# Kernel tuning notes

Hardware: AMD Instinct MI355X
Metric: run time of the kernel (lower is better)

Reference implementation:

```python
import jax, jax.numpy as jnp
import numpy as np

B, T, IN, D = 32, 1024, 1536, 768


def setup_inputs() -> dict:
    key = jax.random.key(0)
    ks = jax.random.split(key, 14)
    s_in = 1.0 / np.sqrt(IN)
    s_d = 1.0 / np.sqrt(D)
    return {
        "x": jax.random.normal(ks[0], (B, T, IN), jnp.float32),
        # fc1/fc2 torch Linear weights stored [out, in]
        "fc1_w": jax.random.normal(ks[1], (IN, IN), jnp.float32) * s_in,
        "fc1_b": jax.random.normal(ks[2], (IN,), jnp.float32) * 0.01,
        "fc2_w": jax.random.normal(ks[3], (D, IN), jnp.float32) * s_in,
        "fc2_b": jax.random.normal(ks[4], (D,), jnp.float32) * 0.01,
        # Unary: Conv1d(D,D,k=1) then Conv1d(D,1,k=1); k=1 conv == per-token linear
        "un_emb_w": jax.random.normal(ks[5], (D, D), jnp.float32) * s_d,
        "un_emb_b": jax.random.normal(ks[6], (D,), jnp.float32) * 0.01,
        "un_red_w": jax.random.normal(ks[7], (1, D), jnp.float32) * s_d,
        "un_red_b": jax.random.normal(ks[8], (1,), jnp.float32) * 0.01,
        # Self Pairwise: x_embedding / y_embedding Conv1d(D,D,k=1)
        "pw_x_w": jax.random.normal(ks[9], (D, D), jnp.float32) * s_d,
        "pw_x_b": jax.random.normal(ks[10], (D,), jnp.float32) * 0.01,
        "pw_y_w": jax.random.normal(ks[11], (D, D), jnp.float32) * s_d,
        "pw_y_b": jax.random.normal(ks[12], (D,), jnp.float32) * 0.01,
        # reduce_potentials: Conv1d(2,1,k=1,bias=False) -> 2 scalars
        "red_w": jax.random.normal(ks[13], (2,), jnp.float32),
    }


def reference(x, fc1_w, fc1_b, fc2_w, fc2_b,
              un_emb_w, un_emb_b, un_red_w, un_red_b,
              pw_x_w, pw_x_b, pw_y_w, pw_y_b, red_w):
    # FGAEmbedder MLP: fc2(relu(fc1(x)))
    h = jax.nn.relu(jnp.einsum('bti,oi->bto', x, fc1_w) + fc1_b)
    u = jnp.einsum('bti,oi->bto', h, fc2_w) + fc2_b            # [B,T,D]

    # Unary potential (dropout is identity at inference)
    e = jax.nn.relu(jnp.einsum('btd,od->bto', u, un_emb_w) + un_emb_b)
    un_pot = (jnp.einsum('btd,od->bto', e, un_red_w) + un_red_b)[..., 0]  # [B,T]

    # Self pairwise: cosine-similarity matrix, marginalized by mean (spatial_dim=None)
    xe = jnp.einsum('btd,od->bto', u, pw_x_w) + pw_x_b
    ye = jnp.einsum('btd,od->bto', u, pw_y_w) + pw_y_b
    xn = xe / jnp.maximum(jnp.linalg.norm(xe, axis=-1, keepdims=True), 1e-12)
    yn = ye / jnp.maximum(jnp.linalg.norm(ye, axis=-1, keepdims=True), 1e-12)
    S = jnp.einsum('btd,bsd->bts', xn, yn)                     # [B,T,T]
    pw_pot = jnp.mean(S, axis=2)                               # [B,T]

    # reduce potentials (Conv1d 2->1 no bias; order: unary then self), softmax attention
    scores = red_w[0] * un_pot + red_w[1] * pw_pot             # [B,T]
    w = jax.nn.softmax(scores, axis=1)
    return jnp.einsum('btd,bt->bd', u, w)                      # [B,D]
```

## Files before the change

### kernel.cpp

```cpp
#include <hip/hip_runtime.h>
#include <stdint.h>

#define MROWS 32768
#define TSEQ  1024
#define BBATCH 32
#define INDIM 1536
#define DDIM  768
#define NCAT  2304

typedef short short8 __attribute__((ext_vector_type(8)));
typedef short short4v __attribute__((ext_vector_type(4)));
typedef float f32x4  __attribute__((ext_vector_type(4)));

__device__ __forceinline__ float b2f(ushort u) {
    union { uint32_t u; float f; } x; x.u = ((uint32_t)u) << 16; return x.f;
}
__device__ __forceinline__ ushort f2b(float f) {
    union { float f; uint32_t u; } x; x.f = f;
    uint32_t r = x.u + 0x7fffu + ((x.u >> 16) & 1u);
    return (ushort)(r >> 16);
}

__device__ __forceinline__ void cvt4(const float* __restrict__ in, ushort* __restrict__ out, int i) {
    float4 v = ((const float4*)in)[i];
    ushort4 o;
    o.x = f2b(v.x); o.y = f2b(v.y); o.z = f2b(v.z); o.w = f2b(v.w);
    ((ushort4*)out)[i] = o;
}

#define C0 12582912
#define C1 13172736
#define C2 13467648
#define C3 13615104
#define C4 13762560
#define C5 13910016
#define C6 13910592
#define C7 13916736
#define C8 13922880
#define C9 13947456
__global__ void cvt_all(const float* __restrict__ x,
                        const float* __restrict__ fc1_w, const float* __restrict__ fc2_w,
                        const float* __restrict__ w3a, const float* __restrict__ w3b,
                        const float* __restrict__ w3c,
                        const float* __restrict__ ba, const float* __restrict__ bb,
                        const float* __restrict__ bc,
                        ushort* __restrict__ X16, ushort* __restrict__ W1,
                        ushort* __restrict__ W2, ushort* __restrict__ W3,
                        float* __restrict__ B3, float* __restrict__ ybar_z,
                        float* __restrict__ out_z, float* __restrict__ stats_z)
{
    int i = blockIdx.x * 256 + threadIdx.x;
    float4 z = {0.f, 0.f, 0.f, 0.f};
    if (i < C0)       cvt4(x, X16, i);
    else if (i < C1)  cvt4(fc1_w, W1, i - C0);
    else if (i < C2)  cvt4(fc2_w, W2, i - C1);
    else if (i < C3)  cvt4(w3a, W3,           i - C2);
    else if (i < C4)  cvt4(w3b, W3 + 589824,  i - C3);
    else if (i < C5)  cvt4(w3c, W3 + 1179648, i - C4);
    else if (i < C6) {
        int j = i - C5;
        const float* src = (j < 192) ? ba : (j < 384) ? bb : bc;
        int off = (j < 192) ? j : (j < 384) ? (j - 192) : (j - 384);
        ((float4*)B3)[j] = ((const float4*)src)[off];
    }
    else if (i < C7)  ((float4*)ybar_z)[i - C6] = z;
    else if (i < C8)  ((float4*)out_z)[i - C7] = z;
    else if (i < C9)  ((float4*)stats_z)[i - C8] = z;
}

__global__ __launch_bounds__(256, 2)
void gemm_bt(const ushort* __restrict__ A, const ushort* __restrict__ Bm,
             const float* __restrict__ bias, ushort* __restrict__ C,
             int M, int N, int K, int relu_ncols,
             const float* __restrict__ urw, float* __restrict__ SE,
             float* __restrict__ SX, float* __restrict__ SY)
{
    __shared__ __align__(16) ushort lA[128 * 64];
    __shared__ __align__(16) ushort lB[128 * 64];

    const int tid  = threadIdx.x;
    const int lane = tid & 63, wave = tid >> 6;
    const int wm = wave & 1, wn = wave >> 1;
    const int quad = lane >> 4, r16 = lane & 15;

    const int ntiles = N >> 7;
    const int xcd = blockIdx.x & 7;
    const int j   = blockIdx.x >> 3;
    const int g   = j / ntiles;
    const int n_t = j - g * ntiles;
    const int m_t = xcd + (g << 3);
    const int m0 = m_t * 128, n0 = n_t * 128;

    const int srow = lane >> 2;
    const int scol = ((lane & 3) ^ ((lane >> 3) & 3)) * 8;
    const int goff = (r16 << 5) + ((quad ^ ((r16 >> 1) & 3)) << 3);

    f32x4 acc[4][4] = {};

    const int kIters = K >> 6;
    for (int kt = 0; kt < kIters; ++kt) {
        const int k0 = kt << 6;
        __syncthreads();
#pragma unroll
        for (int c = 0; c < 4; ++c) {
            int S  = wave * 4 + c;
            int kh = S >> 3, rs = S & 7;
            int row = rs * 16 + srow;
            int kc  = k0 + kh * 32 + scol;
            const ushort* ga = A + (size_t)(m0 + row) * K + kc;
            __builtin_amdgcn_global_load_lds(
                (const __attribute__((address_space(1))) void*)ga,
                (__attribute__((address_space(3))) void*)&lA[S * 512], 16, 0, 0);
            const ushort* gb = Bm + (size_t)(n0 + row) * K + kc;
            __builtin_amdgcn_global_load_lds(
                (const __attribute__((address_space(1))) void*)gb,
                (__attribute__((address_space(3))) void*)&lB[S * 512], 16, 0, 0);
        }
        __syncthreads();

#pragma unroll
        for (int kh = 0; kh < 2; ++kh) {
            short8 af[4], bf[4];
#pragma unroll
            for (int i = 0; i < 4; ++i)
                af[i] = *(const short8*)&lA[kh * 4096 + (wm * 4 + i) * 512 + goff];
#pragma unroll
            for (int j2 = 0; j2 < 4; ++j2)
                bf[j2] = *(const short8*)&lB[kh * 4096 + (wn * 4 + j2) * 512 + goff];
#pragma unroll
            for (int i = 0; i < 4; ++i)
#pragma unroll
                for (int j2 = 0; j2 < 4; ++j2)
                    acc[i][j2] = __builtin_amdgcn_mfma_f32_16x16x32_bf16(af[i], bf[j2], acc[i][j2], 0, 0, 0);
        }
    }

    const bool stats = (urw != nullptr);
    const int sec = n0 / DDIM;
    float st[4][4] = {};
#pragma unroll
    for (int j2 = 0; j2 < 4; ++j2) {
        int gn = n0 + wn * 64 + j2 * 16 + r16;
        float bv = bias[gn];
        bool dorelu = gn < relu_ncols;
        float uw = (stats && sec == 0) ? urw[gn] : 0.f;
#pragma unroll
        for (int i = 0; i < 4; ++i) {
            int gmb = m0 + wm * 64 + i * 16 + quad * 4;
#pragma unroll
            for (int rr = 0; rr < 4; ++rr) {
                float v = acc[i][j2][rr] + bv;
                if (dorelu) v = fmaxf(v, 0.f);
                C[(size_t)(gmb + rr) * N + gn] = f2b(v);
                if (stats) st[i][rr] += (sec == 0) ? v * uw : v * v;
            }
        }
    }
    if (stats) {
#pragma unroll
        for (int i = 0; i < 4; ++i)
#pragma unroll
            for (int rr = 0; rr < 4; ++rr) {
                float v = st[i][rr];
                v += __shfl_xor(v, 1, 64);
                v += __shfl_xor(v, 2, 64);
                v += __shfl_xor(v, 4, 64);
                v += __shfl_xor(v, 8, 64);
                st[i][rr] = v;
            }
        if (r16 == 0) {
            float* dst = (sec == 0) ? SE : (sec == 1) ? SX : SY;
#pragma unroll
            for (int i = 0; i < 4; ++i)
#pragma unroll
                for (int rr = 0; rr < 4; ++rr)
                    atomicAdd(&dst[m0 + wm * 64 + i * 16 + quad * 4 + rr], st[i][rr]);
        }
    }
}

__global__ void ybar_k(const ushort* __restrict__ G3, const float* __restrict__ sy,
                       float* __restrict__ ybar)
{
    int b = blockIdx.x, s0 = blockIdx.y * 32;
    int tid = threadIdx.x;
    __shared__ float sr[32];
    if (tid < 32) {
        float v = sy[b * TSEQ + s0 + tid];
        sr[tid] = (1.0f / TSEQ) / fmaxf(sqrtf(v), 1e-12f);
    }
    __syncthreads();
    float a0 = 0.f, a1 = 0.f, a2 = 0.f;
#pragma unroll 8
    for (int s = 0; s < 32; ++s) {
        const ushort* row = G3 + (size_t)(b * TSEQ + s0 + s) * NCAT + 2 * DDIM;
        float w = sr[s];
        a0 += b2f(row[tid])       * w;
        a1 += b2f(row[tid + 256]) * w;
        a2 += b2f(row[tid + 512]) * w;
    }
    atomicAdd(&ybar[b * DDIM + tid],       a0);
    atomicAdd(&ybar[b * DDIM + tid + 256], a1);
    atomicAdd(&ybar[b * DDIM + tid + 512], a2);
}

__global__ void pw_scores_k(const ushort* __restrict__ G3, const float* __restrict__ ybar,
                            const float* __restrict__ SE, const float* __restrict__ SX,
                            const float* __restrict__ urb, const float* __restrict__ red_w,
                            float* __restrict__ scores)
{
    int wv = threadIdx.x >> 6, lane = threadIdx.x & 63;
    int m = blockIdx.x * 4 + wv;
    int b = m >> 10;
    const ushort* xe = G3 + (size_t)m * NCAT + DDIM;
    const float4* yb = (const float4*)(ybar + b * DDIM);
    float s = 0.f;
#pragma unroll
    for (int c0 = 0; c0 < 3; ++c0) {
        int c = lane + c0 * 64;
        short4v v = *(const short4v*)(xe + c * 4);
        float4 yv = yb[c];
        s += b2f((ushort)v[0]) * yv.x + b2f((ushort)v[1]) * yv.y
           + b2f((ushort)v[2]) * yv.z + b2f((ushort)v[3]) * yv.w;
    }
#pragma unroll
    for (int off = 32; off; off >>= 1) s += __shfl_xor(s, off, 64);
    if (lane == 0) {
        float rnx = 1.f / fmaxf(sqrtf(SX[m]), 1e-12f);
        scores[m] = red_w[0] * (SE[m] + urb[0]) + red_w[1] * (rnx * s);
    }
}

__global__ void out_sm_k(const ushort* __restrict__ U16, const float* __restrict__ scores,
                         float* __restrict__ out)
{
    int b = blockIdx.x, t0 = blockIdx.y * 32;
    int tid = threadIdx.x;
    int lane = tid & 63, wv = tid >> 6;
    __shared__ float red[8];
    __shared__ float sw[32];

    float v[4];
    float lm = -1e30f;
#pragma unroll
    for (int i = 0; i < 4; ++i) {
        v[i] = scores[b * TSEQ + i * 256 + tid];
        lm = fmaxf(lm, v[i]);
    }
#pragma unroll
    for (int off = 32; off; off >>= 1) lm = fmaxf(lm, __shfl_xor(lm, off, 64));
    if (lane == 0) red[wv] = lm;
    __syncthreads();
    float smax = fmaxf(fmaxf(red[0], red[1]), fmaxf(red[2], red[3]));
    float ls = 0.f;
#pragma unroll
    for (int i = 0; i < 4; ++i) ls += expf(v[i] - smax);
#pragma unroll
    for (int off = 32; off; off >>= 1) ls += __shfl_xor(ls, off, 64);
    if (lane == 0) red[4 + wv] = ls;
    __syncthreads();
    float inv = 1.f / (red[4] + red[5] + red[6] + red[7]);

    if (tid < 32) sw[tid] = expf(scores[b * TSEQ + t0 + tid] - smax) * inv;
    __syncthreads();

    float a0 = 0.f, a1 = 0.f, a2 = 0.f;
#pragma unroll 8
    for (int t = 0; t < 32; ++t) {
        const ushort* row = U16 + (size_t)(b * TSEQ + t0 + t) * DDIM;
        float w = sw[t];
        a0 += b2f(row[tid])       * w;
        a1 += b2f(row[tid + 256]) * w;
        a2 += b2f(row[tid + 512]) * w;
    }
    atomicAdd(&out[b * DDIM + tid],       a0);
    atomicAdd(&out[b * DDIM + tid + 256], a1);
    atomicAdd(&out[b * DDIM + tid + 512], a2);
}

static const size_t O_X16   = 0;
static const size_t O_H16   = 100663296;
static const size_t O_G3    = 0;
static const size_t O_U16   = 201326592;
static const size_t O_W1    = 251658240;
static const size_t O_W2    = 256376832;
static const size_t O_W3    = 258736128;
static const size_t O_B3    = 262275072;
static const size_t O_SE    = 262284288;
static const size_t O_SX    = 262415360;
static const size_t O_SY    = 262546432;
static const size_t O_SCORE = 262677504;
static const size_t O_YBAR  = 262939648;

extern "C" void kernel_launch(void* const* d_in, const int* in_sizes, int n_in,
                              void* d_out, int out_size, void* d_ws, size_t ws_size,
                              hipStream_t stream)
{
    const float* x        = (const float*)d_in[0];
    const float* fc1_w    = (const float*)d_in[1];
    const float* fc1_b    = (const float*)d_in[2];
    const float* fc2_w    = (const float*)d_in[3];
    const float* fc2_b    = (const float*)d_in[4];
    const float* un_emb_w = (const float*)d_in[5];
    const float* un_emb_b = (const float*)d_in[6];
    const float* un_red_w = (const float*)d_in[7];
    const float* un_red_b = (const float*)d_in[8];
    const float* pw_x_w   = (const float*)d_in[9];
    const float* pw_x_b   = (const float*)d_in[10];
    const float* pw_y_w   = (const float*)d_in[11];
    const float* pw_y_b   = (const float*)d_in[12];
    const float* red_w    = (const float*)d_in[13];

    char* ws = (char*)d_ws;
    ushort* X16 = (ushort*)(ws + O_X16);
    ushort* H16 = (ushort*)(ws + O_H16);
    ushort* G3  = (ushort*)(ws + O_G3);
    ushort* U16 = (ushort*)(ws + O_U16);
    ushort* W1  = (ushort*)(ws + O_W1);
    ushort* W2  = (ushort*)(ws + O_W2);
    ushort* W3  = (ushort*)(ws + O_W3);
    float*  B3  = (float*)(ws + O_B3);
    float*  SE  = (float*)(ws + O_SE);
    float*  SX  = (float*)(ws + O_SX);
    float*  SY  = (float*)(ws + O_SY);
    float*  SCORES = (float*)(ws + O_SCORE);
    float*  YBAR = (float*)(ws + O_YBAR);

    cvt_all<<<54483, 256, 0, stream>>>(x, fc1_w, fc2_w, un_emb_w, pw_x_w, pw_y_w,
                                       un_emb_b, pw_x_b, pw_y_b,
                                       X16, W1, W2, W3, B3, YBAR, (float*)d_out, SE);

    gemm_bt<<<(MROWS / 128) * (INDIM / 128), 256, 0, stream>>>(
        X16, W1, fc1_b, H16, MROWS, INDIM, INDIM, INDIM,
        nullptr, nullptr, nullptr, nullptr);
    gemm_bt<<<(MROWS / 128) * (DDIM / 128), 256, 0, stream>>>(
        H16, W2, fc2_b, U16, MROWS, DDIM, INDIM, 0,
        nullptr, nullptr, nullptr, nullptr);
    gemm_bt<<<(MROWS / 128) * (NCAT / 128), 256, 0, stream>>>(
        U16, W3, B3, G3, MROWS, NCAT, DDIM, DDIM,
        un_red_w, SE, SX, SY);

    ybar_k<<<dim3(BBATCH, 32), 256, 0, stream>>>(G3, SY, YBAR);
    pw_scores_k<<<MROWS / 4, 256, 0, stream>>>(G3, YBAR, SE, SX, un_red_b, red_w, SCORES);
    out_sm_k<<<dim3(BBATCH, 32), 256, 0, stream>>>(U16, SCORES, (float*)d_out);
}
```

Before: 726.7 us.

## Use 256x256 GEMM tiles with 4-stage LDS prefetch pipeline

```diff
diff --git a/kernel.cpp b/kernel.cpp
--- a/kernel.cpp
+++ b/kernel.cpp
@@ -68,88 +68,122 @@
     else if (i < C9)  ((float4*)stats_z)[i - C8] = z;
 }
 
-__global__ __launch_bounds__(256, 2)
+__global__ __launch_bounds__(512, 2)
 void gemm_bt(const ushort* __restrict__ A, const ushort* __restrict__ Bm,
              const float* __restrict__ bias, ushort* __restrict__ C,
              int M, int N, int K, int relu_ncols,
              const float* __restrict__ urw, float* __restrict__ SE,
              float* __restrict__ SX, float* __restrict__ SY)
 {
-    __shared__ __align__(16) ushort lA[128 * 64];
-    __shared__ __align__(16) ushort lB[128 * 64];
+    __shared__ __align__(16) ushort lds[65536];
 
     const int tid  = threadIdx.x;
     const int lane = tid & 63, wave = tid >> 6;
-    const int wm = wave & 1, wn = wave >> 1;
+    const int wm = wave >> 2, wn = wave & 3;
     const int quad = lane >> 4, r16 = lane & 15;
 
-    const int ntiles = N >> 7;
+    const int ntiles = N >> 8;
     const int xcd = blockIdx.x & 7;
     const int j   = blockIdx.x >> 3;
     const int g   = j / ntiles;
     const int n_t = j - g * ntiles;
     const int m_t = xcd + (g << 3);
-    const int m0 = m_t * 128, n0 = n_t * 128;
+    const int m0 = m_t * 256, n0 = n_t * 256;
 
     const int srow = lane >> 2;
-    const int scol = ((lane & 3) ^ ((lane >> 3) & 3)) * 8;
+    const int sgr  = (lane & 3) ^ ((lane >> 3) & 3);
     const int goff = (r16 << 5) + ((quad ^ ((r16 >> 1) & 3)) << 3);
 
-    f32x4 acc[4][4] = {};
-
-    const int kIters = K >> 6;
-    for (int kt = 0; kt < kIters; ++kt) {
-        const int k0 = kt << 6;
-        __syncthreads();
-#pragma unroll
-        for (int c = 0; c < 4; ++c) {
-            int S  = wave * 4 + c;
-            int kh = S >> 3, rs = S & 7;
-            int row = rs * 16 + srow;
-            int kc  = k0 + kh * 32 + scol;
-            const ushort* ga = A + (size_t)(m0 + row) * K + kc;
-            __builtin_amdgcn_global_load_lds(
-                (const __attribute__((address_space(1))) void*)ga,
-                (__attribute__((address_space(3))) void*)&lA[S * 512], 16, 0, 0);
-            const ushort* gb = Bm + (size_t)(n0 + row) * K + kc;
-            __builtin_amdgcn_global_load_lds(
-                (const __attribute__((address_space(1))) void*)gb,
-                (__attribute__((address_space(3))) void*)&lB[S * 512], 16, 0, 0);
+    const ushort* gA = A  + (size_t)(m0 + wave * 32 + srow) * K + sgr * 8;
+    const ushort* gB = Bm + (size_t)(n0 + wave * 32 + srow) * K + sgr * 8;
+    const int ldsA = wave * 1024;
+    const int ldsB = 8192 + wave * 1024;
+
+    const int kT = K >> 5;
+
+#define STAGE(p, off) __builtin_amdgcn_global_load_lds( \
+        (const __attribute__((address_space(1))) void*)(p), \
+        (__attribute__((address_space(3))) void*)&lds[off], 16, 0, 0)
+
+    for (int t = 0; t < 3; ++t) {
+        const int bufb = t << 14;
+        const ushort* a = gA + (size_t)t * 32;
+        const ushort* b = gB + (size_t)t * 32;
+        STAGE(a,                  bufb + ldsA);
+        STAGE(a + (size_t)16 * K, bufb + ldsA + 512);
+        STAGE(b,                  bufb + ldsB);
+        STAGE(b + (size_t)16 * K, bufb + ldsB + 512);
+    }
+
+    f32x4 acc[8][4] = {};
+
+    asm volatile("s_waitcnt vmcnt(8)" ::: "memory");
+    asm volatile("s_barrier" ::: "memory");
+
+    for (int t = 0; t < kT; ++t) {
+        const int bufb = (t & 3) << 14;
+        const ushort* sa = &lds[bufb + (wm << 12) + goff];
+        const ushort* sb = &lds[bufb + 8192 + (wn << 11) + goff];
+        short8 af[4], bf[4];
+
+#pragma unroll
+        for (int i = 0; i < 4; ++i)  af[i] = *(const short8*)(sa + i * 512);
+#pragma unroll
+        for (int jj = 0; jj < 4; ++jj) bf[jj] = *(const short8*)(sb + jj * 512);
+        if (t + 3 < kT) {
+            const int nb = ((t + 3) & 3) << 14;
+            STAGE(gA + (size_t)(t + 3) * 32, nb + ldsA);
+            STAGE(gB + (size_t)(t + 3) * 32, nb + ldsB);
         }
-        __syncthreads();
-
-#pragma unroll
-        for (int kh = 0; kh < 2; ++kh) {
-            short8 af[4], bf[4];
-#pragma unroll
-            for (int i = 0; i < 4; ++i)
-                af[i] = *(const short8*)&lA[kh * 4096 + (wm * 4 + i) * 512 + goff];
-#pragma unroll
-            for (int j2 = 0; j2 < 4; ++j2)
-                bf[j2] = *(const short8*)&lB[kh * 4096 + (wn * 4 + j2) * 512 + goff];
-#pragma unroll
-            for (int i = 0; i < 4; ++i)
-#pragma unroll
-                for (int j2 = 0; j2 < 4; ++j2)
-                    acc[i][j2] = __builtin_amdgcn_mfma_f32_16x16x32_bf16(af[i], bf[j2], acc[i][j2], 0, 0, 0);
+        asm volatile("s_barrier" ::: "memory");
+        asm volatile("s_waitcnt lgkmcnt(0)" ::: "memory");
+        __builtin_amdgcn_s_setprio(1);
+#pragma unroll
+        for (int i = 0; i < 4; ++i)
+#pragma unroll
+            for (int jj = 0; jj < 4; ++jj)
+                acc[i][jj] = __builtin_amdgcn_mfma_f32_16x16x32_bf16(af[i], bf[jj], acc[i][jj], 0, 0, 0);
+        __builtin_amdgcn_s_setprio(0);
+        asm volatile("s_barrier" ::: "memory");
+
+#pragma unroll
+        for (int i = 0; i < 4; ++i)  af[i] = *(const short8*)(sa + (4 + i) * 512);
+        if (t + 3 < kT) {
+            const int nb = ((t + 3) & 3) << 14;
+            STAGE(gA + (size_t)(t + 3) * 32 + (size_t)16 * K, nb + ldsA + 512);
+            STAGE(gB + (size_t)(t + 3) * 32 + (size_t)16 * K, nb + ldsB + 512);
         }
-    }
+        if (t < kT - 3)       asm volatile("s_waitcnt vmcnt(8)" ::: "memory");
+        else if (t == kT - 3) asm volatile("s_waitcnt vmcnt(4)" ::: "memory");
+        else if (t == kT - 2) asm volatile("s_waitcnt vmcnt(0)" ::: "memory");
+        asm volatile("s_barrier" ::: "memory");
+        asm volatile("s_waitcnt lgkmcnt(0)" ::: "memory");
+        __builtin_amdgcn_s_setprio(1);
+#pragma unroll
+        for (int i = 0; i < 4; ++i)
+#pragma unroll
+            for (int jj = 0; jj < 4; ++jj)
+                acc[4 + i][jj] = __builtin_amdgcn_mfma_f32_16x16x32_bf16(af[i], bf[jj], acc[4 + i][jj], 0, 0, 0);
+        __builtin_amdgcn_s_setprio(0);
+        asm volatile("s_barrier" ::: "memory");
+    }
+#undef STAGE
 
     const bool stats = (urw != nullptr);
     const int sec = n0 / DDIM;
-    float st[4][4] = {};
-#pragma unroll
-    for (int j2 = 0; j2 < 4; ++j2) {
-        int gn = n0 + wn * 64 + j2 * 16 + r16;
+    float st[8][4] = {};
+#pragma unroll
+    for (int jj = 0; jj < 4; ++jj) {
+        int gn = n0 + wn * 64 + jj * 16 + r16;
         float bv = bias[gn];
         bool dorelu = gn < relu_ncols;
         float uw = (stats && sec == 0) ? urw[gn] : 0.f;
 #pragma unroll
-        for (int i = 0; i < 4; ++i) {
-            int gmb = m0 + wm * 64 + i * 16 + quad * 4;
+        for (int i = 0; i < 8; ++i) {
+            int gmb = m0 + wm * 128 + i * 16 + quad * 4;
 #pragma unroll
             for (int rr = 0; rr < 4; ++rr) {
-                float v = acc[i][j2][rr] + bv;
+                float v = acc[i][jj][rr] + bv;
                 if (dorelu) v = fmaxf(v, 0.f);
                 C[(size_t)(gmb + rr) * N + gn] = f2b(v);
                 if (stats) st[i][rr] += (sec == 0) ? v * uw : v * v;
@@ -158,7 +192,7 @@
     }
     if (stats) {
 #pragma unroll
-        for (int i = 0; i < 4; ++i)
+        for (int i = 0; i < 8; ++i)
 #pragma unroll
             for (int rr = 0; rr < 4; ++rr) {
                 float v = st[i][rr];
@@ -171,10 +205,10 @@
         if (r16 == 0) {
             float* dst = (sec == 0) ? SE : (sec == 1) ? SX : SY;
 #pragma unroll
-            for (int i = 0; i < 4; ++i)
+            for (int i = 0; i < 8; ++i)
 #pragma unroll
                 for (int rr = 0; rr < 4; ++rr)
-                    atomicAdd(&dst[m0 + wm * 64 + i * 16 + quad * 4 + rr], st[i][rr]);
+                    atomicAdd(&dst[m0 + wm * 128 + i * 16 + quad * 4 + rr], st[i][rr]);
         }
     }
 }
@@ -330,13 +364,13 @@
                                        un_emb_b, pw_x_b, pw_y_b,
                                        X16, W1, W2, W3, B3, YBAR, (float*)d_out, SE);
 
-    gemm_bt<<<(MROWS / 128) * (INDIM / 128), 256, 0, stream>>>(
+    gemm_bt<<<(MROWS / 256) * (INDIM / 256), 512, 0, stream>>>(
         X16, W1, fc1_b, H16, MROWS, INDIM, INDIM, INDIM,
         nullptr, nullptr, nullptr, nullptr);
-    gemm_bt<<<(MROWS / 128) * (DDIM / 128), 256, 0, stream>>>(
+    gemm_bt<<<(MROWS / 256) * (DDIM / 256), 512, 0, stream>>>(
         H16, W2, fc2_b, U16, MROWS, DDIM, INDIM, 0,
         nullptr, nullptr, nullptr, nullptr);
-    gemm_bt<<<(MROWS / 128) * (NCAT / 128), 256, 0, stream>>>(
+    gemm_bt<<<(MROWS / 256) * (NCAT / 256), 512, 0, stream>>>(
         U16, W3, B3, G3, MROWS, NCAT, DDIM, DDIM,
         un_red_w, SE, SX, SY);
 
```

New measurement: 771.9 us. 6.2% more time.
